# Performance work log

Measured on AMD Instinct MI355X. Metric: run time of the kernel, lower is better.

The kernel has to match this reference:

```python
import jax, jax.numpy as jnp
import numpy as np

B, L, H, T, C = 4, 256, 768, 16, 6
SIM_THR = 0.0
EPS_LN = 1e-5


def layer_norm(x, g, b):
    m = x.mean(-1, keepdims=True)
    v = ((x - m) ** 2).mean(-1, keepdims=True)
    return (x - m) / jnp.sqrt(v + EPS_LN) * g + b


def setup_inputs() -> dict:
    key = jax.random.key(0)
    ks = jax.random.split(key, 20)
    s = 0.02
    embeddings = jax.random.normal(ks[0], (B, L, H), jnp.float32)
    masks = jnp.ones((B, L, L), jnp.float32)
    asp_st = jax.random.randint(ks[1], (B, T), 0, 12)
    asp_ed = asp_st + jax.random.randint(ks[2], (B, T), 0, 3)
    opi_st = jax.random.randint(ks[3], (B, T), 0, 12)
    opi_ed = opi_st + jax.random.randint(ks[4], (B, T), 0, 3)
    sent_id = jax.random.randint(ks[5], (B, T), 2, 5)
    return {
        "embeddings": embeddings, "masks": masks,
        "asp_st": asp_st, "asp_ed": asp_ed, "opi_st": opi_st, "opi_ed": opi_ed,
        "sent_id": sent_id,
        "edge_embed": jax.random.normal(ks[6], (2, H), jnp.float32) * s,
        "W_tp": jax.random.normal(ks[7], (2 * H + 3, H), jnp.float32) * s,
        "b_tp": jnp.zeros((H,), jnp.float32),
        "W_attn": jax.random.normal(ks[8], (3 * H, 1), jnp.float32) * s,
        "b_attn": jnp.zeros((1,), jnp.float32),
        "W_gat": jax.random.normal(ks[9], (2 * H, H), jnp.float32) * s,
        "b_gat": jnp.zeros((H,), jnp.float32),
        "gamma0": jnp.ones((H,), jnp.float32), "beta0": jnp.zeros((H,), jnp.float32),
        "W1": jax.random.normal(ks[10], (2 * H, L), jnp.float32) * s,
        "bl1": jnp.zeros((L,), jnp.float32),
        "gamma1": jnp.ones((L,), jnp.float32), "beta1": jnp.zeros((L,), jnp.float32),
        "Wc": jax.random.normal(ks[11], (L, C), jnp.float32) * s,
        "bc": jnp.zeros((C,), jnp.float32),
        "Wc1": jax.random.normal(ks[12], (L, 2), jnp.float32) * s,
        "bc1": jnp.zeros((2,), jnp.float32),
    }


def _triplet_enhance(emb_b, a_st, a_ed, o_st, o_ed, sid,
                     edge_embed, W_tp, b_tp, W_attn, b_attn, W_gat, b_gat):
    # emb_b: [L,H]; span ints: [T]
    pos = jnp.arange(L)
    am = (pos[None, :] >= a_st[:, None]) & (pos[None, :] <= a_ed[:, None])  # [T,L]
    om = (pos[None, :] >= o_st[:, None]) & (pos[None, :] <= o_ed[:, None])
    amf = am.astype(emb_b.dtype)
    omf = om.astype(emb_b.dtype)
    asp = (amf @ emb_b) / amf.sum(1, keepdims=True)  # [T,H] span-mean
    opi = (omf @ emb_b) / omf.sum(1, keepdims=True)
    sv = jax.nn.one_hot(sid - 2, 3, dtype=emb_b.dtype)  # [T,3]
    nf = jnp.concatenate([asp, opi, sv], -1) @ W_tp + b_tp  # [T,H]

    # cosine similarity between triplet nodes
    nrm = nf / jnp.maximum(jnp.linalg.norm(nf, axis=-1, keepdims=True), 1e-8)
    sim = nrm @ nrm.T
    eye = jnp.eye(T, dtype=bool)
    ok = (sim > SIM_THR) & ~eye
    m0 = ok & (a_st[:, None] == a_st[None, :]) & (a_ed[:, None] == a_ed[None, :])
    m1 = ok & (o_st[:, None] == o_st[None, :]) & (o_ed[:, None] == o_ed[None, :])
    # edge (i,j): src=i, tgt=j -> incoming mask indexed [tgt, src, etype]
    emask = jnp.stack([m0.T, m1.T], axis=-1)  # [T,T,2]

    E = edge_embed  # [2,H]
    cc = jnp.concatenate([
        jnp.broadcast_to(nf[:, None, None, :], (T, T, 2, H)),   # target feats
        jnp.broadcast_to(nf[None, :, None, :], (T, T, 2, H)),   # source feats
        jnp.broadcast_to(E[None, None, :, :], (T, T, 2, H)),
    ], -1)  # [T,T,2,3H]
    scores = (jax.nn.leaky_relu(cc, 0.2) @ W_attn)[..., 0] + b_attn[0]  # [T,T,2]
    neg = jnp.where(emask, scores, -1e9)
    attn = jax.nn.softmax(neg.reshape(T, -1), axis=-1).reshape(T, T, 2)
    msg = jnp.concatenate([
        jnp.broadcast_to(nf[:, None, :], (T, 2, H)),
        jnp.broadcast_to(E[None, :, :], (T, 2, H)),
    ], -1)  # [src, etype, 2H]
    agg = jnp.einsum('tse,sef->tf', attn, msg)
    upd = jax.nn.relu(agg @ W_gat + b_gat)
    has_in = emask.any(axis=(1, 2))
    new_nf = jnp.where(has_in[:, None], upd, nf)
    has_edges = emask.any().astype(emb_b.dtype)  # original skips scatter if no edges
    center = (a_st + o_st) // 2
    return emb_b.at[center].add(new_nf * has_edges)


def reference(embeddings, masks, asp_st, asp_ed, opi_st, opi_ed, sent_id,
              edge_embed, W_tp, b_tp, W_attn, b_attn, W_gat, b_gat,
              gamma0, beta0, W1, bl1, gamma1, beta1, Wc, bc, Wc1, bc1):
    emb1 = layer_norm(embeddings, gamma0, beta0)
    emb = jax.vmap(_triplet_enhance,
                   in_axes=(0, 0, 0, 0, 0, 0) + (None,) * 7)(
        emb1, asp_st, asp_ed, opi_st, opi_ed, sent_id,
        edge_embed, W_tp, b_tp, W_attn, b_attn, W_gat, b_gat)

    # cat([feat_exp, feat_expT]) @ W1  ==  emb@W1[:H] (rows) + emb@W1[H:] (cols)
    A = jnp.einsum('bih,hk->bik', emb, W1[:H])
    Bm = jnp.einsum('bjh,hk->bjk', emb, W1[H:])
    hidden = A[:, :, None, :] + Bm[:, None, :, :] + bl1  # [B,L,L,L]
    hidden = jax.nn.gelu(layer_norm(hidden, gamma1, beta1), approximate=False)
    logits = (hidden @ Wc + bc) * masks[..., None]    # [B,L,L,C]
    logits1 = (hidden @ Wc1 + bc1) * masks[..., None]  # [B,L,L,2]
    return jnp.concatenate([logits, logits1], -1)
```

## Files before the change

### kernel.cpp

```cpp
#include <hip/hip_runtime.h>

__device__ __forceinline__ unsigned short f2bf(float f) {
    union { float f; unsigned u; } v; v.f = f;
    unsigned u = v.u;
    unsigned r = (u + 0x7fffu + ((u >> 16) & 1u)) >> 16;
    return (unsigned short)r;
}
__device__ __forceinline__ float bfup(int x) {
    union { unsigned u; float f; } v; v.u = ((unsigned)(unsigned short)x) << 16; return v.f;
}

typedef __attribute__((ext_vector_type(8))) short short8;
typedef __attribute__((ext_vector_type(4))) float floatx4;

#define Bn 4
#define Ln 256
#define Hn 768
#define Tn 16
#define PITCH 288

__global__ __launch_bounds__(256) void k_pre(const float* __restrict__ x,
                                             const float* __restrict__ g,
                                             const float* __restrict__ be,
                                             float* __restrict__ out,
                                             const float* __restrict__ W1,
                                             unsigned short* __restrict__ w1t,
                                             const float* __restrict__ Wc,
                                             const float* __restrict__ Wc1,
                                             const float* __restrict__ g1,
                                             const float* __restrict__ b1,
                                             unsigned short* __restrict__ wfg,
                                             const int* __restrict__ ast_, const int* __restrict__ aed_,
                                             const int* __restrict__ ost_, const int* __restrict__ oed_,
                                             const int* __restrict__ sid_,
                                             float* __restrict__ xv,
                                             float* __restrict__ nf) {
    int bid = blockIdx.x, tid = threadIdx.x;
    if (bid < 1024) {
        int row = bid;
        const float* xr = x + (size_t)row * Hn;
        float v0 = xr[tid], v1 = xr[tid + 256], v2 = xr[tid + 512];
        float s = v0 + v1 + v2;
        float q = v0 * v0 + v1 * v1 + v2 * v2;
        __shared__ float sm[4], qm[4];
        for (int o = 32; o > 0; o >>= 1) { s += __shfl_down(s, o); q += __shfl_down(q, o); }
        if ((tid & 63) == 0) { sm[tid >> 6] = s; qm[tid >> 6] = q; }
        __syncthreads();
        float S = sm[0] + sm[1] + sm[2] + sm[3];
        float Q = qm[0] + qm[1] + qm[2] + qm[3];
        float mean = S * (1.f / 768.f);
        float rstd = rsqrtf(Q * (1.f / 768.f) - mean * mean + 1e-5f);
        float* o0 = out + (size_t)row * Hn;
        o0[tid]       = (v0 - mean) * rstd * g[tid]       + be[tid];
        o0[tid + 256] = (v1 - mean) * rstd * g[tid + 256] + be[tid + 256];
        o0[tid + 512] = (v2 - mean) * rstd * g[tid + 512] + be[tid + 512];
    } else if (bid < 1408) {
        __shared__ float tile[32][33];
        int idx = bid - 1024;
        int kt = idx % 24, nt = idx / 24;
        int k0 = kt * 32, n0 = nt * 32;
        int rowoff = (n0 < 256) ? 0 : 768;
        int col0 = n0 & 255;
        int r = tid >> 3, c = (tid & 7) * 4;
        float4 v = *(const float4*)(W1 + (size_t)(rowoff + k0 + r) * 256 + col0 + c);
        tile[r][c] = v.x; tile[r][c + 1] = v.y; tile[r][c + 2] = v.z; tile[r][c + 3] = v.w;
        __syncthreads();
        ushort4 o;
        o.x = f2bf(tile[c][r]); o.y = f2bf(tile[c + 1][r]);
        o.z = f2bf(tile[c + 2][r]); o.w = f2bf(tile[c + 3][r]);
        *(ushort4*)(w1t + (size_t)(n0 + r) * 768 + k0 + c) = o;
    } else if (bid == 1408) {
#pragma unroll
        for (int u = 0; u < 2; ++u) {
            int e = tid + u * 256;
            int s = e >> 6, l = e & 63;
            int qq2 = l >> 4, nn2 = l & 15;
            short8 wv;
#pragma unroll
            for (int t = 0; t < 8; ++t) {
                int k = s * 32 + qq2 * 8 + t;
                float v = (nn2 < 6) ? Wc[k * 6 + nn2] : ((nn2 < 8) ? Wc1[k * 2 + (nn2 - 6)] : 0.f);
                wv[t] = (short)f2bf(v);
            }
            *(short8*)(wfg + e * 8) = wv;
        }
        wfg[4096 + tid] = f2bf(g1[tid]);
        wfg[4352 + tid] = f2bf(b1[tid]);
    } else {
        __shared__ float rstdA[3], rstdO[3], cc[2];
        __shared__ float sred[4], qred[4];
        int n = bid - 1409, b = n >> 4;
        int ast = ast_[n], aed = aed_[n], ost = ost_[n], oed = oed_[n], sid = sid_[n];
        int na = aed - ast + 1, no2 = oed - ost + 1;
        if (tid == 0) { cc[0] = 0.f; cc[1] = 0.f; }
        __syncthreads();
        for (int slot = 0; slot < 6; ++slot) {
            int isA = slot < 3;
            int off = isA ? slot : slot - 3;
            int cnt = isA ? na : no2;
            int row = (isA ? ast : ost) + off;
            if (off < cnt) {
                const float* xr = x + (size_t)(b * 256 + row) * Hn;
                float v0 = xr[tid], v1 = xr[tid + 256], v2 = xr[tid + 512];
                float s = v0 + v1 + v2;
                float q = v0 * v0 + v1 * v1 + v2 * v2;
                for (int o = 32; o > 0; o >>= 1) { s += __shfl_down(s, o); q += __shfl_down(q, o); }
                if ((tid & 63) == 0) { sred[tid >> 6] = s; qred[tid >> 6] = q; }
            }
            __syncthreads();
            if (off < cnt && tid == 0) {
                float S = sred[0] + sred[1] + sred[2] + sred[3];
                float Q = qred[0] + qred[1] + qred[2] + qred[3];
                float mean = S * (1.f / 768.f);
                float rstd = rsqrtf(Q * (1.f / 768.f) - mean * mean + 1e-5f);
                if (isA) { rstdA[off] = rstd; cc[0] += mean * rstd; }
                else     { rstdO[off] = rstd; cc[1] += mean * rstd; }
            }
            __syncthreads();
        }
        float ai = 1.f / (float)na, oi = 1.f / (float)no2;
        float cA = cc[0] * ai, cO = cc[1] * oi;
        float* xrr = xv + (size_t)n * 1568;
        const float* eb = x + (size_t)b * Ln * Hn;
        for (int r = tid; r < 1568; r += 256) {
            float v;
            if (r < 768) {
                float sa = 0.f;
                for (int l = 0; l < na; ++l) sa = fmaf(eb[(ast + l) * Hn + r], rstdA[l], sa);
                v = fmaf(g[r], sa * ai - cA, be[r]);
            } else if (r < 1536) {
                int h = r - 768;
                float so = 0.f;
                for (int l = 0; l < no2; ++l) so = fmaf(eb[(ost + l) * Hn + h], rstdO[l], so);
                v = fmaf(g[h], so * oi - cO, be[h]);
            } else if (r < 1539) {
                v = (sid - 2 == r - 1536) ? 1.f : 0.f;
            } else {
                v = 0.f;
            }
            xrr[r] = v;
        }
        float* nr = nf + (size_t)n * Hn;
        nr[tid] = 0.f; nr[tid + 256] = 0.f; nr[tid + 512] = 0.f;
    }
}

__global__ __launch_bounds__(256) void k_skinny(const float* __restrict__ A,
                                                const float* __restrict__ B,
                                                const float* __restrict__ bias,
                                                float* __restrict__ C,
                                                int Kpad, int Kb, int Kc) {
    __shared__ float At[32][33], Bt[32][33];
    int tid = threadIdx.x;
    int n0 = blockIdx.x * 32, m0 = blockIdx.y * 32, z = blockIdx.z;
    int kbeg = z * Kc;
    int kend = kbeg + Kc; if (kend > Kpad) kend = Kpad;
    int lr = tid >> 3, lc = (tid & 7) * 4;
    int tm = tid >> 3, tn4 = (tid & 7) * 4;
    float acc0 = 0.f, acc1 = 0.f, acc2 = 0.f, acc3 = 0.f;
    for (int k0 = kbeg; k0 < kend; k0 += 32) {
        float4 av = *(const float4*)(A + (size_t)(m0 + lr) * Kpad + k0 + lc);
        At[lr][lc] = av.x; At[lr][lc + 1] = av.y; At[lr][lc + 2] = av.z; At[lr][lc + 3] = av.w;
        int gk = k0 + lr;
        float4 bv = {0.f, 0.f, 0.f, 0.f};
        if (gk < Kb) bv = *(const float4*)(B + (size_t)gk * 768 + n0 + lc);
        Bt[lr][lc] = bv.x; Bt[lr][lc + 1] = bv.y; Bt[lr][lc + 2] = bv.z; Bt[lr][lc + 3] = bv.w;
        __syncthreads();
#pragma unroll
        for (int k = 0; k < 32; ++k) {
            float a = At[tm][k];
            acc0 = fmaf(a, Bt[k][tn4], acc0);
            acc1 = fmaf(a, Bt[k][tn4 + 1], acc1);
            acc2 = fmaf(a, Bt[k][tn4 + 2], acc2);
            acc3 = fmaf(a, Bt[k][tn4 + 3], acc3);
        }
        __syncthreads();
    }
    if (z == 0) {
        acc0 += bias[n0 + tn4];
        acc1 += bias[n0 + tn4 + 1];
        acc2 += bias[n0 + tn4 + 2];
        acc3 += bias[n0 + tn4 + 3];
    }
    float* dst = C + (size_t)(m0 + tm) * 768 + n0 + tn4;
    atomicAdd(&dst[0], acc0);
    atomicAdd(&dst[1], acc1);
    atomicAdd(&dst[2], acc2);
    atomicAdd(&dst[3], acc3);
}

__global__ __launch_bounds__(256) void k_graph(const float* __restrict__ nf,
                                               const int* __restrict__ ast_, const int* __restrict__ aed_,
                                               const int* __restrict__ ost_, const int* __restrict__ oed_,
                                               const float* __restrict__ E,
                                               const float* __restrict__ Wat,
                                               const float* __restrict__ bat,
                                               int* __restrict__ hasin, float* __restrict__ hasedge,
                                               float* __restrict__ agg, float* __restrict__ raw) {
    int b = blockIdx.x, tid = threadIdx.x;
    __shared__ float nfs[16][780];
    __shared__ float Es[2][768];
    __shared__ int ast[16], aed[16], ost[16], oed[16];
    __shared__ float red[256];
    __shared__ float nrm[16], p[16], q[16], rr[2];
    __shared__ float ws2[16][16];
    __shared__ float aes[16][2];
    __shared__ unsigned m0b[16], m1b[16];
    const float* nfb = nf + (size_t)b * 16 * Hn;
    for (int e = tid; e < 3072; e += 256) {
        int r = e / 192, c = (e - r * 192) * 4;
        float4 v = *(const float4*)(nfb + r * Hn + c);
        nfs[r][c] = v.x; nfs[r][c + 1] = v.y; nfs[r][c + 2] = v.z; nfs[r][c + 3] = v.w;
    }
    for (int e = tid; e < 1536; e += 256) ((float*)Es)[e] = E[e];
    if (tid < 16) {
        int n = b * 16 + tid;
        ast[tid] = ast_[n]; aed[tid] = aed_[n]; ost[tid] = ost_[n]; oed[tid] = oed_[n];
        m0b[tid] = 0u; m1b[tid] = 0u;
    }
    __syncthreads();
    int t = tid >> 4, lane = tid & 15;
    float ss = 0.f, pp = 0.f, qq = 0.f;
    for (int h = lane; h < 768; h += 16) {
        float v = nfs[t][h];
        ss = fmaf(v, v, ss);
        float lr = v > 0.f ? v : 0.2f * v;
        pp = fmaf(lr, Wat[h], pp);
        qq = fmaf(lr, Wat[768 + h], qq);
    }
    red[tid] = ss; __syncthreads();
    if (tid < 16) { float s = 0.f; for (int k2 = 0; k2 < 16; ++k2) s += red[tid * 16 + k2]; nrm[tid] = sqrtf(s); }
    __syncthreads();
    red[tid] = pp; __syncthreads();
    if (tid < 16) { float s = 0.f; for (int k2 = 0; k2 < 16; ++k2) s += red[tid * 16 + k2]; p[tid] = s; }
    __syncthreads();
    red[tid] = qq; __syncthreads();
    if (tid < 16) { float s = 0.f; for (int k2 = 0; k2 < 16; ++k2) s += red[tid * 16 + k2]; q[tid] = s; }
    __syncthreads();
    float rp = 0.f;
    if (tid < 32) {
        int e = tid >> 4;
        for (int h = lane; h < 768; h += 16) {
            float v = Es[e][h];
            float lr = v > 0.f ? v : 0.2f * v;
            rp = fmaf(lr, Wat[1536 + h], rp);
        }
    }
    red[tid] = rp; __syncthreads();
    if (tid < 2) { float s = 0.f; for (int k2 = 0; k2 < 16; ++k2) s += red[tid * 16 + k2]; rr[tid] = s; }
    __syncthreads();
    {
        int i = tid >> 4, j = tid & 15;
        const float4* ri = (const float4*)nfs[i];
        const float4* rj = (const float4*)nfs[j];
        float dot = 0.f;
#pragma unroll 4
        for (int h4 = 0; h4 < 192; ++h4) {
            float4 a = ri[h4], c = rj[h4];
            dot = fmaf(a.x, c.x, dot); dot = fmaf(a.y, c.y, dot);
            dot = fmaf(a.z, c.z, dot); dot = fmaf(a.w, c.w, dot);
        }
        float sim = dot / (fmaxf(nrm[i], 1e-8f) * fmaxf(nrm[j], 1e-8f));
        bool ok = (sim > 0.f) && (i != j);
        if (ok && ast[i] == ast[j] && aed[i] == aed[j]) atomicOr(&m0b[i], 1u << j);
        if (ok && ost[i] == ost[j] && oed[i] == oed[j]) atomicOr(&m1b[i], 1u << j);
    }
    __syncthreads();
    if (tid < 16) {
        int tt = tid;
        float battn = bat[0];
        float sc[32];
        float mx = -3.4e38f;
        bool hi = false;
#pragma unroll
        for (int s = 0; s < 16; ++s) {
            bool e0 = (m0b[s] >> tt) & 1u;
            bool e1 = (m1b[s] >> tt) & 1u;
            float base = p[tt] + q[s] + battn;
            float v0 = e0 ? (base + rr[0]) : -1e9f;
            float v1 = e1 ? (base + rr[1]) : -1e9f;
            sc[2 * s] = v0; sc[2 * s + 1] = v1;
            mx = fmaxf(mx, fmaxf(v0, v1));
            hi = hi || e0 || e1;
        }
        float sum = 0.f;
#pragma unroll
        for (int k2 = 0; k2 < 32; ++k2) { float e = expf(sc[k2] - mx); sc[k2] = e; sum += e; }
        float inv = 1.f / sum;
        float ae0 = 0.f, ae1 = 0.f;
#pragma unroll
        for (int s = 0; s < 16; ++s) {
            float w0 = sc[2 * s] * inv, w1 = sc[2 * s + 1] * inv;
            ws2[tt][s] = w0 + w1;
            ae0 += w0; ae1 += w1;
        }
        aes[tt][0] = ae0; aes[tt][1] = ae1;
        hasin[b * 16 + tt] = hi ? 1 : 0;
        red[tid] = hi ? 1.f : 0.f;
    }
    __syncthreads();
    if (tid == 0) {
        float he = 0.f;
        for (int k2 = 0; k2 < 16; ++k2) he = fmaxf(he, red[k2]);
        hasedge[b] = he;
    }
    for (int nn = 0; nn < 16; ++nn) {
        int n = b * 16 + nn;
        float ae0 = aes[nn][0], ae1 = aes[nn][1];
        float* ag = agg + (size_t)n * 1536;
        float* rw = raw + (size_t)n * Hn;
        for (int f = tid; f < 768; f += 256) {
            float s = 0.f;
#pragma unroll
            for (int s16 = 0; s16 < 16; ++s16) s = fmaf(ws2[nn][s16], nfs[s16][f], s);
            ag[f] = s;
            ag[768 + f] = ae0 * Es[0][f] + ae1 * Es[1][f];
            rw[f] = 0.f;
        }
    }
}

__global__ __launch_bounds__(256) void k_scatter(const float* __restrict__ raw,
                                                 const float* __restrict__ nf,
                                                 const int* __restrict__ hasin, const float* __restrict__ hasedge,
                                                 const int* __restrict__ ast_, const int* __restrict__ ost_,
                                                 float* __restrict__ emb) {
    int n = blockIdx.x, b = n >> 4, tid = threadIdx.x;
    if (hasedge[b] == 0.f) return;
    int center = (ast_[n] + ost_[n]) >> 1;
    float* dst = emb + (size_t)(b * Ln + center) * Hn;
    int hi = hasin[n];
    const float* src = hi ? (raw + (size_t)n * Hn) : (nf + (size_t)n * Hn);
    for (int h = tid; h < 768; h += 256) {
        float v = src[h];
        if (hi) v = fmaxf(v, 0.f);
        atomicAdd(&dst[h], v);
    }
}

__global__ __launch_bounds__(64) void k_gemm(const float* __restrict__ emb,
                                             const unsigned short* __restrict__ w1t,
                                             float* __restrict__ abm) {
    int wid = blockIdx.x;
    int m0 = (wid >> 4) * 32;
    int n0 = (wid & 15) * 32;
    int lane = threadIdx.x;
    int r = lane & 15, g = lane >> 4;
    const float* Af0 = emb + (size_t)(m0 + r) * 768 + g * 8;
    const float* Af1 = emb + (size_t)(m0 + 16 + r) * 768 + g * 8;
    const short8* Bp0 = (const short8*)(w1t + (size_t)(n0 + r) * 768 + g * 8);
    const short8* Bp1 = (const short8*)(w1t + (size_t)(n0 + 16 + r) * 768 + g * 8);
    floatx4 acc00 = {0.f, 0.f, 0.f, 0.f}, acc01 = {0.f, 0.f, 0.f, 0.f};
    floatx4 acc10 = {0.f, 0.f, 0.f, 0.f}, acc11 = {0.f, 0.f, 0.f, 0.f};
#pragma unroll 4
    for (int ks = 0; ks < 768; ks += 32) {
        float4 x0 = *(const float4*)(Af0 + ks);
        float4 x1 = *(const float4*)(Af0 + ks + 4);
        float4 y0 = *(const float4*)(Af1 + ks);
        float4 y1 = *(const float4*)(Af1 + ks + 4);
        short8 a0, a1;
        union { float f; unsigned u; } cv;
#define PK(dst, idx, val) { cv.f = (val); dst[idx] = (short)((cv.u + 0x8000u) >> 16); }
        PK(a0, 0, x0.x) PK(a0, 1, x0.y) PK(a0, 2, x0.z) PK(a0, 3, x0.w)
        PK(a0, 4, x1.x) PK(a0, 5, x1.y) PK(a0, 6, x1.z) PK(a0, 7, x1.w)
        PK(a1, 0, y0.x) PK(a1, 1, y0.y) PK(a1, 2, y0.z) PK(a1, 3, y0.w)
        PK(a1, 4, y1.x) PK(a1, 5, y1.y) PK(a1, 6, y1.z) PK(a1, 7, y1.w)
#undef PK
        short8 b0 = Bp0[ks >> 3];
        short8 b1 = Bp1[ks >> 3];
        acc00 = __builtin_amdgcn_mfma_f32_16x16x32_bf16(a0, b0, acc00, 0, 0, 0);
        acc01 = __builtin_amdgcn_mfma_f32_16x16x32_bf16(a0, b1, acc01, 0, 0, 0);
        acc10 = __builtin_amdgcn_mfma_f32_16x16x32_bf16(a1, b0, acc10, 0, 0, 0);
        acc11 = __builtin_amdgcn_mfma_f32_16x16x32_bf16(a1, b1, acc11, 0, 0, 0);
    }
#pragma unroll
    for (int t = 0; t < 4; ++t) {
        int row = g * 4 + t;
        abm[(size_t)(m0 + row) * 512 + n0 + r]           = acc00[t];
        abm[(size_t)(m0 + row) * 512 + n0 + 16 + r]      = acc01[t];
        abm[(size_t)(m0 + 16 + row) * 512 + n0 + r]      = acc10[t];
        abm[(size_t)(m0 + 16 + row) * 512 + n0 + 16 + r] = acc11[t];
    }
}

__global__ __launch_bounds__(256) void k_hidden3(const float* __restrict__ abm,
                                                 const float* __restrict__ bl1,
                                                 const float* __restrict__ masks,
                                                 const unsigned short* __restrict__ wfg,
                                                 const float* __restrict__ bc,
                                                 const float* __restrict__ bc1,
                                                 float* __restrict__ out) {
    __shared__ unsigned short As[16][PITCH];
    __shared__ unsigned short Bs[16][PITCH];
    __shared__ unsigned short gsh[256], bsh[256];
    __shared__ short8 Wf[8][64];
    __shared__ float Ds[16][16];
    __shared__ float ms[16][16];
    __shared__ float sAs[16], qAs[16], sBs[16], qBs[16];
    int tid = threadIdx.x;
    int jt = blockIdx.x, it = blockIdx.y, b = blockIdx.z;
    int rowA = b * 256 + it * 16;
    int rowB = b * 256 + jt * 16;
    {
        int r = tid >> 4, sg = tid & 15;
        const float* Ar = abm + (size_t)(rowA + r) * 512 + sg * 16;
        const float* Br = abm + (size_t)(rowB + r) * 512 + 256 + sg * 16;
        const float* Lr = bl1 + sg * 16;
        float sa = 0.f, qa = 0.f, sb = 0.f, qb = 0.f;
        short8 va0, va1, vb0, vb1;
#pragma unroll
        for (int u = 0; u < 4; ++u) {
            float4 av = *(const float4*)(Ar + u * 4);
            float4 bv = *(const float4*)(Br + u * 4);
            float4 lv = *(const float4*)(Lr + u * 4);
            float aa[4] = {av.x, av.y, av.z, av.w};
            float bb[4] = {bv.x + lv.x, bv.y + lv.y, bv.z + lv.z, bv.w + lv.w};
#pragma unroll
            for (int e = 0; e < 4; ++e) {
                unsigned short ah = f2bf(aa[e]), bh = f2bf(bb[e]);
                float af = bfup(ah), bf2 = bfup(bh);
                sa += af; qa = fmaf(af, af, qa);
                sb += bf2; qb = fmaf(bf2, bf2, qb);
                int pos = u * 4 + e;
                if (pos < 8) { va0[pos] = (short)ah; vb0[pos] = (short)bh; }
                else         { va1[pos - 8] = (short)ah; vb1[pos - 8] = (short)bh; }
            }
        }
        *(short8*)&As[r][sg * 16]     = va0;
        *(short8*)&As[r][sg * 16 + 8] = va1;
        *(short8*)&Bs[r][sg * 16]     = vb0;
        *(short8*)&Bs[r][sg * 16 + 8] = vb1;
        for (int o = 8; o > 0; o >>= 1) {
            sa += __shfl_down(sa, o); qa += __shfl_down(qa, o);
            sb += __shfl_down(sb, o); qb += __shfl_down(qb, o);
        }
        if (sg == 0) { sAs[r] = sa; qAs[r] = qa; sBs[r] = sb; qBs[r] = qb; }
    }
#pragma unroll
    for (int u = 0; u < 2; ++u) {
        int e = tid + u * 256;
        ((short8*)Wf)[e] = *(const short8*)(wfg + e * 8);
    }
    gsh[tid] = wfg[4096 + tid];
    bsh[tid] = wfg[4352 + tid];
    {
        int di = tid >> 4, dj = tid & 15;
        ms[di][dj] = masks[((size_t)(b * 256 + it * 16 + di)) * 256 + jt * 16 + dj];
    }
    __syncthreads();
    if (tid < 64) {
        int m = tid & 15, q = tid >> 4;
        floatx4 acc = {0.f, 0.f, 0.f, 0.f};
#pragma unroll
        for (int s = 0; s < 8; ++s) {
            short8 a8 = *(const short8*)&As[m][s * 32 + q * 8];
            short8 b8 = *(const short8*)&Bs[m][s * 32 + q * 8];
            acc = __builtin_amdgcn_mfma_f32_16x16x32_bf16(a8, b8, acc, 0, 0, 0);
        }
#pragma unroll
        for (int rg = 0; rg < 4; ++rg) Ds[q * 4 + rg][m] = acc[rg];
    }
    __syncthreads();

    int lane = tid & 63, w = tid >> 6;
    int m = lane & 15, q = lane >> 4;
    int iA = w * 4 + (m & 3);
    int jB0 = m >> 2;
    int n = m;
    float bcs_l = (n < 6) ? bc[n] : ((n < 8) ? bc1[n - 6] : 0.f);
    const float inv256 = 1.f / 256.f;
    const float K1 = -1.5957691216f, K2 = -0.0713548163f;

    float rr4[4], cc4[4];
#pragma unroll
    for (int p = 0; p < 4; ++p) {
        int jB = p * 4 + jB0;
        float mu = (sAs[iA] + sBs[jB]) * inv256;
        float E2 = (qAs[iA] + 2.f * Ds[iA][jB] + qBs[jB]) * inv256;
        float r_ = rsqrtf(E2 - mu * mu + 1e-5f);
        rr4[p] = r_;
        cc4[p] = -mu * r_;
    }
    floatx4 acc0 = {0.f, 0.f, 0.f, 0.f};
    floatx4 acc1 = {0.f, 0.f, 0.f, 0.f};
    floatx4 acc2 = {0.f, 0.f, 0.f, 0.f};
    floatx4 acc3 = {0.f, 0.f, 0.f, 0.f};

#pragma unroll 2
    for (int s = 0; s < 8; ++s) {
        int ko = s * 32 + q * 8;
        short8 a8 = *(const short8*)&As[iA][ko];
        short8 g8 = *(const short8*)&gsh[ko];
        short8 v8 = *(const short8*)&bsh[ko];
        short8 wv = Wf[s][lane];
        float af[8], gf[8], vf[8];
#pragma unroll
        for (int t = 0; t < 8; ++t) { af[t] = bfup(a8[t]); gf[t] = bfup(g8[t]); vf[t] = bfup(v8[t]); }
#define PSTEP(P, ACC) do {                                                        \
        short8 b8 = *(const short8*)&Bs[P * 4 + jB0][ko];                         \
        float r_ = rr4[P], c_ = cc4[P];                                           \
        short8 yv;                                                                \
        _Pragma("unroll")                                                         \
        for (int t = 0; t < 8; ++t) {                                             \
            float x = fmaf(af[t] + bfup(b8[t]), r_, c_);                          \
            x = fmaf(x, gf[t], vf[t]);                                            \
            float mm = fmaf(x * x, K2, K1);                                       \
            float e = __expf(x * mm);                                             \
            float y = x * __builtin_amdgcn_rcpf(1.f + e);                         \
            union { float f; unsigned u; } cv; cv.f = y;                          \
            yv[t] = (short)((cv.u + 0x8000u) >> 16);                              \
        }                                                                         \
        ACC = __builtin_amdgcn_mfma_f32_16x16x32_bf16(yv, wv, ACC, 0, 0, 0);      \
    } while (0)
        PSTEP(0, acc0);
        PSTEP(1, acc1);
        PSTEP(2, acc2);
        PSTEP(3, acc3);
#undef PSTEP
    }

    if (n < 8) {
#pragma unroll
        for (int rg = 0; rg < 4; ++rg) {
            int mp = q * 4 + rg;
            int il = w * 4 + (mp & 3);
            int base_j = mp >> 2;
            size_t rowbase = ((size_t)(b * 256 + it * 16 + il)) * 256 + jt * 16;
            {
                int jl = 0 * 4 + base_j;
                out[(rowbase + jl) * 8 + n] = (acc0[rg] + bcs_l) * ms[il][jl];
            }
            {
                int jl = 1 * 4 + base_j;
                out[(rowbase + jl) * 8 + n] = (acc1[rg] + bcs_l) * ms[il][jl];
            }
            {
                int jl = 2 * 4 + base_j;
                out[(rowbase + jl) * 8 + n] = (acc2[rg] + bcs_l) * ms[il][jl];
            }
            {
                int jl = 3 * 4 + base_j;
                out[(rowbase + jl) * 8 + n] = (acc3[rg] + bcs_l) * ms[il][jl];
            }
        }
    }
}

extern "C" void kernel_launch(void* const* d_in, const int* in_sizes, int n_in,
                              void* d_out, int out_size, void* d_ws, size_t ws_size,
                              hipStream_t stream) {
    (void)in_sizes; (void)n_in; (void)out_size; (void)ws_size;
    const float* emb_in = (const float*)d_in[0];
    const float* masks  = (const float*)d_in[1];
    const int* ast = (const int*)d_in[2];
    const int* aed = (const int*)d_in[3];
    const int* ost = (const int*)d_in[4];
    const int* oed = (const int*)d_in[5];
    const int* sid = (const int*)d_in[6];
    const float* E    = (const float*)d_in[7];
    const float* Wtp  = (const float*)d_in[8];
    const float* btp  = (const float*)d_in[9];
    const float* Wat  = (const float*)d_in[10];
    const float* bat  = (const float*)d_in[11];
    const float* Wg   = (const float*)d_in[12];
    const float* bg   = (const float*)d_in[13];
    const float* g0   = (const float*)d_in[14];
    const float* b0   = (const float*)d_in[15];
    const float* W1   = (const float*)d_in[16];
    const float* bl1  = (const float*)d_in[17];
    const float* g1   = (const float*)d_in[18];
    const float* b1   = (const float*)d_in[19];
    const float* Wc   = (const float*)d_in[20];
    const float* bc   = (const float*)d_in[21];
    const float* Wc1  = (const float*)d_in[22];
    const float* bc1  = (const float*)d_in[23];
    float* outp = (float*)d_out;

    float* fw = (float*)d_ws;
    float* emb = fw;
    float* nf  = fw + 786432;
    int*   hasin = (int*)(fw + 835584);
    float* hasedge = fw + 835648;
    float* xv  = fw + 835712;
    float* agg = fw + 936064;
    float* raw = fw + 1034368;
    float* abm = fw + 1083520;
    unsigned short* w1t = (unsigned short*)(fw + 1607808);
    unsigned short* wfg = (unsigned short*)(fw + 1804416);

    k_pre<<<1473, 256, 0, stream>>>(emb_in, g0, b0, emb, W1, w1t,
                                    Wc, Wc1, g1, b1, wfg,
                                    ast, aed, ost, oed, sid, xv, nf);
    dim3 gs1(24, 2, 7);
    k_skinny<<<gs1, 256, 0, stream>>>(xv, Wtp, btp, nf, 1568, 1539, 224);
    k_graph<<<4, 256, 0, stream>>>(nf, ast, aed, ost, oed, E, Wat, bat, hasin, hasedge, agg, raw);
    k_skinny<<<gs1, 256, 0, stream>>>(agg, Wg, bg, raw, 1536, 1536, 224);
    k_scatter<<<64, 256, 0, stream>>>(raw, nf, hasin, hasedge, ast, ost, emb);
    k_gemm<<<512, 64, 0, stream>>>(emb, w1t, abm);
    dim3 g6(16, 16, 4);
    k_hidden3<<<g6, 256, 0, stream>>>(abm, bl1, masks, wfg, bc, bc1, outp);
}
```

Measured before the change: 230.5 us.

## Split graph attention kernel into one block per triplet node

The graph kernel previously ran with only 4 blocks, one per batch, and each block did all 16 nodes serially through many barriers. It now launches 64 blocks, one per target node. Each block computes its own dot products, norms and attention scores, runs the softmax with wavefront shuffles, and writes only its own aggregation row. The has-edge flag becomes an atomic count, zeroed in the preprocessing kernel. In exchange, each block reloads the 16 node features of its batch, so global reads are duplicated 16 times.

```diff
diff --git a/kernel.cpp b/kernel.cpp
--- a/kernel.cpp
+++ b/kernel.cpp
@@ -18,6 +18,7 @@
 #define Hn 768
 #define Tn 16
 #define PITCH 288
+#define PN 784
 
 __global__ __launch_bounds__(256) void k_pre(const float* __restrict__ x,
                                              const float* __restrict__ g,
@@ -34,7 +35,8 @@
                                              const int* __restrict__ ost_, const int* __restrict__ oed_,
                                              const int* __restrict__ sid_,
                                              float* __restrict__ xv,
-                                             float* __restrict__ nf) {
+                                             float* __restrict__ nf,
+                                             float* __restrict__ hedge) {
     int bid = blockIdx.x, tid = threadIdx.x;
     if (bid < 1024) {
         int row = bid;
@@ -86,6 +88,7 @@
         }
         wfg[4096 + tid] = f2bf(g1[tid]);
         wfg[4352 + tid] = f2bf(b1[tid]);
+        if (tid < 4) hedge[tid] = 0.f;
     } else {
         __shared__ float rstdA[3], rstdO[3], cc[2];
         __shared__ float sred[4], qred[4];
@@ -197,126 +200,90 @@
                                                const float* __restrict__ bat,
                                                int* __restrict__ hasin, float* __restrict__ hasedge,
                                                float* __restrict__ agg, float* __restrict__ raw) {
-    int b = blockIdx.x, tid = threadIdx.x;
-    __shared__ float nfs[16][780];
-    __shared__ float Es[2][768];
-    __shared__ int ast[16], aed[16], ost[16], oed[16];
-    __shared__ float red[256];
-    __shared__ float nrm[16], p[16], q[16], rr[2];
-    __shared__ float ws2[16][16];
-    __shared__ float aes[16][2];
-    __shared__ unsigned m0b[16], m1b[16];
+    int n = blockIdx.x, b = n >> 4, t = n & 15, tid = threadIdx.x;
+    __shared__ float nfs[16][PN];
+    __shared__ float dotS[16], n2S[16], qS[16];
+    __shared__ float pT_s, rr0_s, rr1_s;
+    __shared__ int asts[16], aeds[16], osts[16], oeds[16];
+    __shared__ float wss[16];
+    __shared__ float aes0, aes1;
     const float* nfb = nf + (size_t)b * 16 * Hn;
-    for (int e = tid; e < 3072; e += 256) {
-        int r = e / 192, c = (e - r * 192) * 4;
-        float4 v = *(const float4*)(nfb + r * Hn + c);
-        nfs[r][c] = v.x; nfs[r][c + 1] = v.y; nfs[r][c + 2] = v.z; nfs[r][c + 3] = v.w;
-    }
-    for (int e = tid; e < 1536; e += 256) ((float*)Es)[e] = E[e];
     if (tid < 16) {
-        int n = b * 16 + tid;
-        ast[tid] = ast_[n]; aed[tid] = aed_[n]; ost[tid] = ost_[n]; oed[tid] = oed_[n];
-        m0b[tid] = 0u; m1b[tid] = 0u;
+        int m = b * 16 + tid;
+        asts[tid] = ast_[m]; aeds[tid] = aed_[m];
+        osts[tid] = ost_[m]; oeds[tid] = oed_[m];
+    }
+    int s = tid >> 4, l = tid & 15;
+    const float* vs = nfb + (size_t)s * Hn;
+    const float* vt = nfb + (size_t)t * Hn;
+    const float* er = E + ((s == 2) ? 768 : 0);
+    float d = 0.f, n2 = 0.f, qq = 0.f, pp = 0.f, rr = 0.f;
+#pragma unroll 4
+    for (int h = l; h < 768; h += 16) {
+        float v = vs[h];
+        float tv = vt[h];
+        nfs[s][h] = v;
+        d  = fmaf(tv, v, d);
+        n2 = fmaf(v, v, n2);
+        float lv = v > 0.f ? v : 0.2f * v;
+        qq = fmaf(lv, Wat[768 + h], qq);
+        if (s == 0) { float lt = tv > 0.f ? tv : 0.2f * tv; pp = fmaf(lt, Wat[h], pp); }
+        if (s == 1 || s == 2) { float ev = er[h]; float le = ev > 0.f ? ev : 0.2f * ev; rr = fmaf(le, Wat[1536 + h], rr); }
+    }
+    for (int o = 8; o > 0; o >>= 1) {
+        d  += __shfl_down(d, o);  n2 += __shfl_down(n2, o);
+        qq += __shfl_down(qq, o); pp += __shfl_down(pp, o);
+        rr += __shfl_down(rr, o);
+    }
+    if (l == 0) {
+        dotS[s] = d; n2S[s] = n2; qS[s] = qq;
+        if (s == 0) pT_s = pp;
+        if (s == 1) rr0_s = rr;
+        if (s == 2) rr1_s = rr;
     }
     __syncthreads();
-    int t = tid >> 4, lane = tid & 15;
-    float ss = 0.f, pp = 0.f, qq = 0.f;
-    for (int h = lane; h < 768; h += 16) {
-        float v = nfs[t][h];
-        ss = fmaf(v, v, ss);
-        float lr = v > 0.f ? v : 0.2f * v;
-        pp = fmaf(lr, Wat[h], pp);
-        qq = fmaf(lr, Wat[768 + h], qq);
-    }
-    red[tid] = ss; __syncthreads();
-    if (tid < 16) { float s = 0.f; for (int k2 = 0; k2 < 16; ++k2) s += red[tid * 16 + k2]; nrm[tid] = sqrtf(s); }
+    if (tid < 64) {
+        int ss = tid >> 1, e = tid & 1;
+        bool valid = tid < 32;
+        int ssc = ss & 15;
+        float nt = sqrtf(n2S[t]);
+        float ns = sqrtf(n2S[ssc]);
+        float sim = dotS[ssc] / (fmaxf(nt, 1e-8f) * fmaxf(ns, 1e-8f));
+        bool ok = valid && (sim > 0.f) && (ssc != t);
+        bool edge;
+        if (e == 0) edge = ok && (asts[t] == asts[ssc]) && (aeds[t] == aeds[ssc]);
+        else        edge = ok && (osts[t] == osts[ssc]) && (oeds[t] == oeds[ssc]);
+        float sc = edge ? (pT_s + qS[ssc] + (e ? rr1_s : rr0_s) + bat[0]) : -1e9f;
+        float mx = sc;
+        for (int o = 16; o > 0; o >>= 1) mx = fmaxf(mx, __shfl_xor(mx, o));
+        float ex = __expf(sc - mx);
+        float sum = ex;
+        for (int o = 16; o > 0; o >>= 1) sum += __shfl_xor(sum, o);
+        float w = ex / sum;
+        float wtot = w + __shfl_xor(w, 1);
+        if (valid && e == 0) wss[ss] = wtot;
+        float a0 = (valid && e == 0) ? w : 0.f;
+        float a1 = (valid && e == 1) ? w : 0.f;
+        for (int o = 16; o > 0; o >>= 1) { a0 += __shfl_xor(a0, o); a1 += __shfl_xor(a1, o); }
+        unsigned long long bal = __ballot(edge);
+        if (tid == 0) {
+            aes0 = a0; aes1 = a1;
+            int hi = (bal != 0ull) ? 1 : 0;
+            hasin[n] = hi;
+            if (hi) atomicAdd(&hasedge[b], 1.f);
+        }
+    }
     __syncthreads();
-    red[tid] = pp; __syncthreads();
-    if (tid < 16) { float s = 0.f; for (int k2 = 0; k2 < 16; ++k2) s += red[tid * 16 + k2]; p[tid] = s; }
-    __syncthreads();
-    red[tid] = qq; __syncthreads();
-    if (tid < 16) { float s = 0.f; for (int k2 = 0; k2 < 16; ++k2) s += red[tid * 16 + k2]; q[tid] = s; }
-    __syncthreads();
-    float rp = 0.f;
-    if (tid < 32) {
-        int e = tid >> 4;
-        for (int h = lane; h < 768; h += 16) {
-            float v = Es[e][h];
-            float lr = v > 0.f ? v : 0.2f * v;
-            rp = fmaf(lr, Wat[1536 + h], rp);
-        }
-    }
-    red[tid] = rp; __syncthreads();
-    if (tid < 2) { float s = 0.f; for (int k2 = 0; k2 < 16; ++k2) s += red[tid * 16 + k2]; rr[tid] = s; }
-    __syncthreads();
-    {
-        int i = tid >> 4, j = tid & 15;
-        const float4* ri = (const float4*)nfs[i];
-        const float4* rj = (const float4*)nfs[j];
-        float dot = 0.f;
-#pragma unroll 4
-        for (int h4 = 0; h4 < 192; ++h4) {
-            float4 a = ri[h4], c = rj[h4];
-            dot = fmaf(a.x, c.x, dot); dot = fmaf(a.y, c.y, dot);
-            dot = fmaf(a.z, c.z, dot); dot = fmaf(a.w, c.w, dot);
-        }
-        float sim = dot / (fmaxf(nrm[i], 1e-8f) * fmaxf(nrm[j], 1e-8f));
-        bool ok = (sim > 0.f) && (i != j);
-        if (ok && ast[i] == ast[j] && aed[i] == aed[j]) atomicOr(&m0b[i], 1u << j);
-        if (ok && ost[i] == ost[j] && oed[i] == oed[j]) atomicOr(&m1b[i], 1u << j);
-    }
-    __syncthreads();
-    if (tid < 16) {
-        int tt = tid;
-        float battn = bat[0];
-        float sc[32];
-        float mx = -3.4e38f;
-        bool hi = false;
-#pragma unroll
-        for (int s = 0; s < 16; ++s) {
-            bool e0 = (m0b[s] >> tt) & 1u;
-            bool e1 = (m1b[s] >> tt) & 1u;
-            float base = p[tt] + q[s] + battn;
-            float v0 = e0 ? (base + rr[0]) : -1e9f;
-            float v1 = e1 ? (base + rr[1]) : -1e9f;
-            sc[2 * s] = v0; sc[2 * s + 1] = v1;
-            mx = fmaxf(mx, fmaxf(v0, v1));
-            hi = hi || e0 || e1;
-        }
-        float sum = 0.f;
-#pragma unroll
-        for (int k2 = 0; k2 < 32; ++k2) { float e = expf(sc[k2] - mx); sc[k2] = e; sum += e; }
-        float inv = 1.f / sum;
-        float ae0 = 0.f, ae1 = 0.f;
-#pragma unroll
-        for (int s = 0; s < 16; ++s) {
-            float w0 = sc[2 * s] * inv, w1 = sc[2 * s + 1] * inv;
-            ws2[tt][s] = w0 + w1;
-            ae0 += w0; ae1 += w1;
-        }
-        aes[tt][0] = ae0; aes[tt][1] = ae1;
-        hasin[b * 16 + tt] = hi ? 1 : 0;
-        red[tid] = hi ? 1.f : 0.f;
-    }
-    __syncthreads();
-    if (tid == 0) {
-        float he = 0.f;
-        for (int k2 = 0; k2 < 16; ++k2) he = fmaxf(he, red[k2]);
-        hasedge[b] = he;
-    }
-    for (int nn = 0; nn < 16; ++nn) {
-        int n = b * 16 + nn;
-        float ae0 = aes[nn][0], ae1 = aes[nn][1];
-        float* ag = agg + (size_t)n * 1536;
-        float* rw = raw + (size_t)n * Hn;
-        for (int f = tid; f < 768; f += 256) {
-            float s = 0.f;
-#pragma unroll
-            for (int s16 = 0; s16 < 16; ++s16) s = fmaf(ws2[nn][s16], nfs[s16][f], s);
-            ag[f] = s;
-            ag[768 + f] = ae0 * Es[0][f] + ae1 * Es[1][f];
-            rw[f] = 0.f;
-        }
+    float ae0 = aes0, ae1 = aes1;
+    float* ag = agg + (size_t)n * 1536;
+    float* rw = raw + (size_t)n * Hn;
+    for (int f = tid; f < 768; f += 256) {
+        float acc = 0.f;
+#pragma unroll
+        for (int s16 = 0; s16 < 16; ++s16) acc = fmaf(wss[s16], nfs[s16][f], acc);
+        ag[f] = acc;
+        ag[768 + f] = ae0 * E[f] + ae1 * E[768 + f];
+        rw[f] = 0.f;
     }
 }
 
@@ -590,10 +557,10 @@
 
     k_pre<<<1473, 256, 0, stream>>>(emb_in, g0, b0, emb, W1, w1t,
                                     Wc, Wc1, g1, b1, wfg,
-                                    ast, aed, ost, oed, sid, xv, nf);
+                                    ast, aed, ost, oed, sid, xv, nf, hasedge);
     dim3 gs1(24, 2, 7);
     k_skinny<<<gs1, 256, 0, stream>>>(xv, Wtp, btp, nf, 1568, 1539, 224);
-    k_graph<<<4, 256, 0, stream>>>(nf, ast, aed, ost, oed, E, Wat, bat, hasin, hasedge, agg, raw);
+    k_graph<<<64, 256, 0, stream>>>(nf, ast, aed, ost, oed, E, Wat, bat, hasin, hasedge, agg, raw);
     k_skinny<<<gs1, 256, 0, stream>>>(agg, Wg, bg, raw, 1536, 1536, 224);
     k_scatter<<<64, 256, 0, stream>>>(raw, nf, hasin, hasedge, ast, ost, emb);
     k_gemm<<<512, 64, 0, stream>>>(emb, w1t, abm);
```

New measurement: 225.7 us. 2.1% less time.
